# Performance work log

Hardware: AMD Instinct MI355X
Metric: run time of the kernel (lower is better)

The kernel has to match this reference:

```python
import jax, jax.numpy as jnp
import numpy as np

B, C_IN, C_OUT, K, H, W = 8, 64, 64, 3, 128, 128
CTX = max(8, C_OUT // 4)  # 16


def setup_inputs() -> dict:
    key = jax.random.key(0)
    ks = jax.random.split(key, 6)
    x = jax.random.normal(ks[0], (B, C_IN, H, W), dtype=jnp.float32)
    # context_proj: 1x1 conv (ctx_ch, C_in) + bias
    ctx_w = jax.random.normal(ks[1], (CTX, C_IN), dtype=jnp.float32) * (1.0 / np.sqrt(C_IN))
    ctx_b = jnp.zeros((CTX,), dtype=jnp.float32)
    # kernel_gen: Linear(ctx_ch -> C_out*C_in*K*K), init std=0.001, zero bias
    kg_w = jax.random.normal(ks[2], (C_OUT * C_IN * K * K, CTX), dtype=jnp.float32) * 0.001
    kg_b = jnp.zeros((C_OUT * C_IN * K * K,), dtype=jnp.float32)
    gamma = jnp.zeros((C_OUT,), dtype=jnp.float32)
    bias = jnp.zeros((C_OUT,), dtype=jnp.float32)
    # value_proj: 1x1 conv (C_in, C_in), no bias
    value_w = jax.random.normal(ks[3], (C_IN, C_IN), dtype=jnp.float32) * (1.0 / np.sqrt(C_IN))
    return {"x": x, "ctx_w": ctx_w, "ctx_b": ctx_b, "kg_w": kg_w, "kg_b": kg_b,
            "gamma": gamma, "bias": bias, "value_w": value_w}


def reference(x, ctx_w, ctx_b, kg_w, kg_b, gamma, bias, value_w):
    b = x.shape[0]
    # context projection (1x1 conv) + global average pool -> (B, CTX)
    ctx = jnp.einsum('bchw,oc->bohw', x, ctx_w) + ctx_b[None, :, None, None]
    ctx_vec = jnp.mean(ctx, axis=(2, 3))  # (B, CTX)
    # per-sample kernel generation
    kernels_flat = ctx_vec @ kg_w.T + kg_b  # (B, O*C*K*K)
    kernels = jnp.tanh(kernels_flat.reshape(b, C_OUT, C_IN, K, K))
    mean_k = jnp.mean(kernels.reshape(b, C_OUT, -1), axis=-1)  # (B, O)
    lam = jax.nn.sigmoid(gamma)[None, :, None, None, None]
    kernels = kernels - lam * mean_k[:, :, None, None, None]
    # value projection (1x1 conv, no bias)
    v = jnp.einsum('bchw,oc->bohw', x, value_w)
    # unfold: patches (B, C*K*K, H, W), feature order (C, kh, kw) matching F.unfold
    pad = K // 2
    patches = jax.lax.conv_general_dilated_patches(
        v, filter_shape=(K, K), window_strides=(1, 1),
        padding=[(pad, pad), (pad, pad)])  # (B, C*K*K, H, W)
    out = jnp.einsum('bof,bfhw->bohw', kernels.reshape(b, C_OUT, -1), patches)
    out = out + bias[None, :, None, None]
    return jax.nn.relu(out)
```

## Files before the change

### kernel.cpp

```cpp
#include <hip/hip_runtime.h>
#include <stdint.h>

#define NB 8
#define CIN 64
#define COUT 64
#define HH 128
#define WW 128

typedef unsigned short ushort_t;
typedef unsigned int uint_t;
typedef __attribute__((ext_vector_type(8))) __bf16 bf16x8;
typedef __attribute__((ext_vector_type(4))) float f32x4;

__device__ __forceinline__ ushort_t f2bf(float f) {
  uint_t u = __builtin_bit_cast(uint_t, f);
  u += 0x7fffu + ((u >> 16) & 1u);
  return (ushort_t)(u >> 16);
}

#define WS_PART 0
#define WS_XT   262144
#define WS_A    17039360

__global__ void k_trans(const float* __restrict__ x, ushort_t* __restrict__ xT,
                        float* __restrict__ part) {
  __shared__ float tile[64 * 129];
  int b = blockIdx.x >> 7;
  int h = blockIdx.x & 127;
  int tid = threadIdx.x;
  int w = tid & 127;
  int ch = tid >> 7;
  const float* xp = x + ((size_t)(b * 64) * 128 + h) * 128 + w;
#pragma unroll
  for (int p = 0; p < 32; ++p) {
    int c = p * 2 + ch;
    tile[c * 129 + w] = xp[(size_t)c * 16384];
  }
  __syncthreads();
  if (tid < 64) {
    float s = 0.f;
#pragma unroll 8
    for (int w2 = 0; w2 < 128; ++w2) s += tile[tid * 129 + w2];
    part[((size_t)b * 128 + h) * 64 + tid] = s;
  }
#pragma unroll
  for (int it = 0; it < 4; ++it) {
    int chunk = tid + it * 256;
    int w2 = chunk >> 3;
    int cc = chunk & 7;
    union { ushort_t u[8]; int4 v; } pk;
#pragma unroll
    for (int j = 0; j < 8; ++j) pk.u[j] = f2bf(tile[(cc * 8 + j) * 129 + w2]);
    *reinterpret_cast<int4*>(xT + (((size_t)(b * 128 + h) * 128 + w2) * 64 + cc * 8)) = pk.v;
  }
}

__global__ void k_gen(const float* __restrict__ part,
                      const float* __restrict__ ctx_w, const float* __restrict__ ctx_b,
                      const float* __restrict__ kg_w, const float* __restrict__ kg_b,
                      const float* __restrict__ gamma, const float* __restrict__ value_w,
                      ushort_t* __restrict__ A) {
  __shared__ float xm[64];
  __shared__ float ctxv[16];
  __shared__ float ks_[576];
  __shared__ float red[256];
  __shared__ float vw[4096];
  int b = blockIdx.x >> 6;
  int o = blockIdx.x & 63;
  int tid = threadIdx.x;
  {
    int c = tid & 63;
    int g = tid >> 6;
    float s = 0.f;
    const float* pp = part + ((size_t)b * 128 + g * 32) * 64 + c;
#pragma unroll 8
    for (int h = 0; h < 32; ++h) s += pp[h * 64];
    red[tid] = s;
  }
#pragma unroll
  for (int p = 0; p < 16; ++p) vw[tid + p * 256] = value_w[tid + p * 256];
  __syncthreads();
  if (tid < 64)
    xm[tid] = (red[tid] + red[tid + 64] + red[tid + 128] + red[tid + 192]) * (1.f / 16384.f);
  __syncthreads();
  if (tid < 16) {
    float s = ctx_b[tid];
#pragma unroll 8
    for (int c = 0; c < 64; ++c) s += xm[c] * ctx_w[tid * 64 + c];
    ctxv[tid] = s;
  }
  __syncthreads();
  float val[3] = {0.f, 0.f, 0.f};
  float partial = 0.f;
#pragma unroll
  for (int p = 0; p < 3; ++p) {
    int i = tid + p * 256;
    if (i < 576) {
      int n = o * 576 + i;
      float s = kg_b[n];
      const float* kwp = kg_w + (size_t)n * 16;
#pragma unroll
      for (int j = 0; j < 16; ++j) s += ctxv[j] * kwp[j];
      val[p] = tanhf(s);
      partial += val[p];
    }
  }
  __syncthreads();
  red[tid] = partial;
  __syncthreads();
  for (int s = 128; s > 0; s >>= 1) {
    if (tid < s) red[tid] += red[tid + s];
    __syncthreads();
  }
  float mean = red[0] * (1.f / 576.f);
  float lam = 1.f / (1.f + expf(-gamma[o]));
#pragma unroll
  for (int p = 0; p < 3; ++p) {
    int i = tid + p * 256;
    if (i < 576) ks_[i] = val[p] - lam * mean;
  }
  __syncthreads();
  ushort_t* Ao = A + (size_t)(b * 64 + o) * 576;
#pragma unroll
  for (int p = 0; p < 3; ++p) {
    int f = tid + p * 256;
    if (f < 576) {
      int tap = f >> 6;
      int c = f & 63;
      float s = 0.f;
#pragma unroll 8
      for (int cp = 0; cp < 64; ++cp) s += ks_[cp * 9 + tap] * vw[cp * 64 + c];
      Ao[f] = f2bf(s);
    }
  }
}

__launch_bounds__(256, 2)
__global__ void k_conv(const ushort_t* __restrict__ xT, const ushort_t* __restrict__ A,
                       const float* __restrict__ bias, float* __restrict__ out) {
  __shared__ __align__(16) ushort_t xs[6 * 34 * 72];
  int bx = blockIdx.x;
  int b = bx >> 7;
  int rem = bx & 127;
  int h0 = (rem >> 2) * 4;
  int w0 = (rem & 3) * 32;
  int tid = threadIdx.x;
  int wave = tid >> 6;
  int lane = tid & 63;
  int n16 = lane & 15;
  int q = lane >> 4;
  int p  = wave & 1;
  int oh = wave >> 1;

  bf16x8 af[2][18];
#pragma unroll
  for (int t = 0; t < 2; ++t) {
    const ushort_t* Ag = A + (size_t)(b * 64 + oh * 32 + t * 16 + n16) * 576 + q * 8;
#pragma unroll
    for (int ks = 0; ks < 18; ++ks)
      af[t][ks] = *reinterpret_cast<const bf16x8*>(Ag + ks * 32);
  }

  const ushort_t* xb = xT + (size_t)b * 128 * 128 * 64;
#pragma unroll
  for (int it = 0; it < 7; ++it) {
    int chunk = tid + it * 256;
    if (chunk < 1632) {
      int lr = chunk / 272;
      int r2 = chunk - lr * 272;
      int lc = r2 >> 3;
      int cc = r2 & 7;
      int hh = h0 - 1 + lr;
      int ww = w0 - 1 + lc;
      int4 v = make_int4(0, 0, 0, 0);
      if (hh >= 0 && hh < 128 && ww >= 0 && ww < 128)
        v = *reinterpret_cast<const int4*>(xb + ((size_t)(hh * 128 + ww) * 64 + cc * 8));
      *reinterpret_cast<int4*>(xs + ((lr * 34 + lc) * 72 + cc * 8)) = v;
    }
  }
  __syncthreads();

  f32x4 acc[4][2];
#pragma unroll
  for (int i = 0; i < 4; ++i)
#pragma unroll
    for (int t = 0; t < 2; ++t) acc[i][t] = (f32x4){0.f, 0.f, 0.f, 0.f};

  const ushort_t* xsl = xs + n16 * 72 + q * 8;
#pragma unroll
  for (int pt = 0; pt < 4; ++pt) {
    int nt = p * 4 + pt;
    int rr = nt >> 1, cb = nt & 1;
#pragma unroll
    for (int tap = 0; tap < 9; ++tap) {
      int kh = tap / 3, kw2 = tap % 3;
#pragma unroll
      for (int cq = 0; cq < 2; ++cq) {
        bf16x8 bf = *reinterpret_cast<const bf16x8*>(
            xsl + ((rr + kh) * 34 + cb * 16 + kw2) * 72 + cq * 32);
        int ks = tap * 2 + cq;
        acc[pt][0] = __builtin_amdgcn_mfma_f32_16x16x32_bf16(af[0][ks], bf, acc[pt][0], 0, 0, 0);
        acc[pt][1] = __builtin_amdgcn_mfma_f32_16x16x32_bf16(af[1][ks], bf, acc[pt][1], 0, 0, 0);
      }
    }
  }

#pragma unroll
  for (int pt = 0; pt < 4; ++pt) {
    int nt = p * 4 + pt;
    int rr = nt >> 1, cb = nt & 1;
    int hcur = h0 + rr;
    int wcur = w0 + cb * 16 + n16;
#pragma unroll
    for (int t = 0; t < 2; ++t) {
#pragma unroll
      for (int r = 0; r < 4; ++r) {
        int o = oh * 32 + t * 16 + q * 4 + r;
        float v = acc[pt][t][r] + bias[o];
        v = fmaxf(v, 0.f);
        out[((size_t)(b * 64 + o) * 128 + hcur) * 128 + wcur] = v;
      }
    }
  }
}

extern "C" void kernel_launch(void* const* d_in, const int* in_sizes, int n_in,
                              void* d_out, int out_size, void* d_ws, size_t ws_size,
                              hipStream_t stream) {
  const float* x       = (const float*)d_in[0];
  const float* ctx_w   = (const float*)d_in[1];
  const float* ctx_b   = (const float*)d_in[2];
  const float* kg_w    = (const float*)d_in[3];
  const float* kg_b    = (const float*)d_in[4];
  const float* gamma   = (const float*)d_in[5];
  const float* bias    = (const float*)d_in[6];
  const float* value_w = (const float*)d_in[7];
  float* out = (float*)d_out;

  float* part  = (float*)((char*)d_ws + WS_PART);
  ushort_t* xT = (ushort_t*)((char*)d_ws + WS_XT);
  ushort_t* A  = (ushort_t*)((char*)d_ws + WS_A);

  k_trans<<<1024, 256, 0, stream>>>(x, xT, part);
  k_gen<<<512, 256, 0, stream>>>(part, ctx_w, ctx_b, kg_w, kg_b, gamma, value_w, A);
  k_conv<<<1024, 256, 0, stream>>>(xT, A, bias, out);
}
```

Measured before the change: 132.0 us.

## Drop bf16 NHWC transpose pass; convert fp32 NCHW directly into LDS in conv

Removes the k_trans kernel that wrote a bf16 channels-last copy of x. A simple per-(b,c) mean-reduction kernel replaces it, and k_conv now reads fp32 NCHW x directly, packs channel pairs to bf16 and writes them into the shared tile, with separate loads for the halo columns. This removes a 16 MB intermediate write and its reread. The cost is more, narrower global loads in the conv kernel (4-byte strided per-channel reads) and conversion work repeated across overlapping tiles. It also leaves a dead no-op block behind.

Measured after the change: 154.9 us. 17.3% more time.

```diff
diff --git a/kernel.cpp b/kernel.cpp
--- a/kernel.cpp
+++ b/kernel.cpp
@@ -18,44 +18,30 @@
   return (ushort_t)(u >> 16);
 }
 
-#define WS_PART 0
-#define WS_XT   262144
-#define WS_A    17039360
-
-__global__ void k_trans(const float* __restrict__ x, ushort_t* __restrict__ xT,
-                        float* __restrict__ part) {
-  __shared__ float tile[64 * 129];
-  int b = blockIdx.x >> 7;
-  int h = blockIdx.x & 127;
+#define WS_A    0
+#define WS_XSUM 589824
+
+__global__ void k_mean(const float* __restrict__ x, float* __restrict__ xsum) {
+  __shared__ float red[256];
+  int bc = blockIdx.x;
   int tid = threadIdx.x;
-  int w = tid & 127;
-  int ch = tid >> 7;
-  const float* xp = x + ((size_t)(b * 64) * 128 + h) * 128 + w;
-#pragma unroll
-  for (int p = 0; p < 32; ++p) {
-    int c = p * 2 + ch;
-    tile[c * 129 + w] = xp[(size_t)c * 16384];
-  }
-  __syncthreads();
-  if (tid < 64) {
-    float s = 0.f;
-#pragma unroll 8
-    for (int w2 = 0; w2 < 128; ++w2) s += tile[tid * 129 + w2];
-    part[((size_t)b * 128 + h) * 64 + tid] = s;
-  }
-#pragma unroll
-  for (int it = 0; it < 4; ++it) {
-    int chunk = tid + it * 256;
-    int w2 = chunk >> 3;
-    int cc = chunk & 7;
-    union { ushort_t u[8]; int4 v; } pk;
-#pragma unroll
-    for (int j = 0; j < 8; ++j) pk.u[j] = f2bf(tile[(cc * 8 + j) * 129 + w2]);
-    *reinterpret_cast<int4*>(xT + (((size_t)(b * 128 + h) * 128 + w2) * 64 + cc * 8)) = pk.v;
-  }
-}
-
-__global__ void k_gen(const float* __restrict__ part,
+  const float4* xp4 = (const float4*)(x + (size_t)bc * 16384);
+  float s = 0.f;
+#pragma unroll
+  for (int i = 0; i < 16; ++i) {
+    float4 v = xp4[tid + i * 256];
+    s += (v.x + v.y) + (v.z + v.w);
+  }
+  red[tid] = s;
+  __syncthreads();
+  for (int st = 128; st > 0; st >>= 1) {
+    if (tid < st) red[tid] += red[tid + st];
+    __syncthreads();
+  }
+  if (tid == 0) xsum[bc] = red[0];
+}
+
+__global__ void k_gen(const float* __restrict__ xsum,
                       const float* __restrict__ ctx_w, const float* __restrict__ ctx_b,
                       const float* __restrict__ kg_w, const float* __restrict__ kg_b,
                       const float* __restrict__ gamma, const float* __restrict__ value_w,
@@ -68,20 +54,9 @@
   int b = blockIdx.x >> 6;
   int o = blockIdx.x & 63;
   int tid = threadIdx.x;
-  {
-    int c = tid & 63;
-    int g = tid >> 6;
-    float s = 0.f;
-    const float* pp = part + ((size_t)b * 128 + g * 32) * 64 + c;
-#pragma unroll 8
-    for (int h = 0; h < 32; ++h) s += pp[h * 64];
-    red[tid] = s;
-  }
+  if (tid < 64) xm[tid] = xsum[b * 64 + tid] * (1.f / 16384.f);
 #pragma unroll
   for (int p = 0; p < 16; ++p) vw[tid + p * 256] = value_w[tid + p * 256];
-  __syncthreads();
-  if (tid < 64)
-    xm[tid] = (red[tid] + red[tid + 64] + red[tid + 128] + red[tid + 192]) * (1.f / 16384.f);
   __syncthreads();
   if (tid < 16) {
     float s = ctx_b[tid];
@@ -105,7 +80,6 @@
       partial += val[p];
     }
   }
-  __syncthreads();
   red[tid] = partial;
   __syncthreads();
   for (int s = 128; s > 0; s >>= 1) {
@@ -136,7 +110,7 @@
 }
 
 __launch_bounds__(256, 2)
-__global__ void k_conv(const ushort_t* __restrict__ xT, const ushort_t* __restrict__ A,
+__global__ void k_conv(const float* __restrict__ x, const ushort_t* __restrict__ A,
                        const float* __restrict__ bias, float* __restrict__ out) {
   __shared__ __align__(16) ushort_t xs[6 * 34 * 72];
   int bx = blockIdx.x;
@@ -161,21 +135,46 @@
       af[t][ks] = *reinterpret_cast<const bf16x8*>(Ag + ks * 32);
   }
 
-  const ushort_t* xb = xT + (size_t)b * 128 * 128 * 64;
-#pragma unroll
-  for (int it = 0; it < 7; ++it) {
+  const float* xb = x + (size_t)b * 64 * 16384;
+#pragma unroll
+  for (int it = 0; it < 24; ++it) {
     int chunk = tid + it * 256;
-    if (chunk < 1632) {
-      int lr = chunk / 272;
-      int r2 = chunk - lr * 272;
-      int lc = r2 >> 3;
-      int cc = r2 & 7;
+    int lcp = chunk & 31;
+    int cp  = (chunk >> 5) & 31;
+    int lr  = chunk >> 10;
+    int hh = h0 - 1 + lr;
+    int ww = w0 + lcp;
+    uint_t pk = 0;
+    if (hh >= 0 && hh < 128) {
+      const float* src = xb + ((size_t)(2 * cp) * 128 + hh) * 128 + ww;
+      float f0 = src[0];
+      float f1 = src[16384];
+      pk = (uint_t)f2bf(f0) | ((uint_t)f2bf(f1) << 16);
+    }
+    *reinterpret_cast<uint_t*>(xs + (lr * 34 + (lcp + 1)) * 72 + 2 * cp) = pk;
+  }
+  {
+    int chunk = tid + ((tid < 128) ? 256 : 0);
+  }
+#pragma unroll
+  for (int it = 0; it < 2; ++it) {
+    int chunk = tid + it * 256;
+    if (chunk < 384) {
+      int side = chunk & 1;
+      int rest = chunk >> 1;
+      int cp = rest & 31;
+      int lr = rest >> 5;
+      int lc = side ? 33 : 0;
       int hh = h0 - 1 + lr;
       int ww = w0 - 1 + lc;
-      int4 v = make_int4(0, 0, 0, 0);
-      if (hh >= 0 && hh < 128 && ww >= 0 && ww < 128)
-        v = *reinterpret_cast<const int4*>(xb + ((size_t)(hh * 128 + ww) * 64 + cc * 8));
-      *reinterpret_cast<int4*>(xs + ((lr * 34 + lc) * 72 + cc * 8)) = v;
+      uint_t pk = 0;
+      if (hh >= 0 && hh < 128 && ww >= 0 && ww < 128) {
+        const float* src = xb + ((size_t)(2 * cp) * 128 + hh) * 128 + ww;
+        float f0 = src[0];
+        float f1 = src[16384];
+        pk = (uint_t)f2bf(f0) | ((uint_t)f2bf(f1) << 16);
+      }
+      *reinterpret_cast<uint_t*>(xs + (lr * 34 + lc) * 72 + 2 * cp) = pk;
     }
   }
   __syncthreads();
@@ -237,11 +236,10 @@
   const float* value_w = (const float*)d_in[7];
   float* out = (float*)d_out;
 
-  float* part  = (float*)((char*)d_ws + WS_PART);
-  ushort_t* xT = (ushort_t*)((char*)d_ws + WS_XT);
   ushort_t* A  = (ushort_t*)((char*)d_ws + WS_A);
-
-  k_trans<<<1024, 256, 0, stream>>>(x, xT, part);
-  k_gen<<<512, 256, 0, stream>>>(part, ctx_w, ctx_b, kg_w, kg_b, gamma, value_w, A);
-  k_conv<<<1024, 256, 0, stream>>>(xT, A, bias, out);
-}
+  float* xsum  = (float*)((char*)d_ws + WS_XSUM);
+
+  k_mean<<<512, 256, 0, stream>>>(x, xsum);
+  k_gen<<<512, 256, 0, stream>>>(xsum, ctx_w, ctx_b, kg_w, kg_b, gamma, value_w, A);
+  k_conv<<<1024, 256, 0, stream>>>(x, A, bias, out);
+}
```

## Pre-pad transposed input, stream A fragments per row, stage output through LDS

Applied to the files above, without the earlier changes.

The transpose kernel now writes a zero-padded 130x130 layout, with extra blocks zeroing the border rows, so the conv halo load needs no bounds checks. The conv kernel stops holding all 36 A fragments in registers and reloads 12 per kernel row inside a non-unrolled loop. It raises launch bounds from 2 to 4 blocks per SIMD. The epilogue stages results through shared memory so each output row is written as coalesced float4 stores. The cost is repeated A loads from global or cache, extra barriers in the epilogue, and a larger workspace.

After: 130.9 us. About the same (-0.9%).

```diff
diff --git a/kernel.cpp b/kernel.cpp
--- a/kernel.cpp
+++ b/kernel.cpp
@@ -20,14 +20,23 @@
 
 #define WS_PART 0
 #define WS_XT   262144
-#define WS_A    17039360
-
-__global__ void k_trans(const float* __restrict__ x, ushort_t* __restrict__ xT,
+#define WS_A    17567744
+
+__global__ void k_trans(const float* __restrict__ x, ushort_t* __restrict__ xTp,
                         float* __restrict__ part) {
+  int bx = blockIdx.x;
+  int tid = threadIdx.x;
+  if (bx >= 1024) {
+    int j = bx - 1024;
+    int b = j >> 1;
+    int row = (j & 1) ? 129 : 0;
+    int4* dst = reinterpret_cast<int4*>(xTp + ((size_t)b * 130 + row) * 130 * 64);
+    for (int it = tid; it < 1040; it += 256) dst[it] = make_int4(0, 0, 0, 0);
+    return;
+  }
   __shared__ float tile[64 * 129];
-  int b = blockIdx.x >> 7;
-  int h = blockIdx.x & 127;
-  int tid = threadIdx.x;
+  int b = bx >> 7;
+  int h = bx & 127;
   int w = tid & 127;
   int ch = tid >> 7;
   const float* xp = x + ((size_t)(b * 64) * 128 + h) * 128 + w;
@@ -43,6 +52,13 @@
     for (int w2 = 0; w2 < 128; ++w2) s += tile[tid * 129 + w2];
     part[((size_t)b * 128 + h) * 64 + tid] = s;
   }
+  if (tid < 16) {
+    int col = (tid < 8) ? 0 : 129;
+    int cc = tid & 7;
+    *reinterpret_cast<int4*>(xTp + (((size_t)b * 130 + h + 1) * 130 + col) * 64 + cc * 8) =
+        make_int4(0, 0, 0, 0);
+  }
+  ushort_t* dst = xTp + (((size_t)b * 130 + h + 1) * 130 + 1) * 64;
 #pragma unroll
   for (int it = 0; it < 4; ++it) {
     int chunk = tid + it * 256;
@@ -51,7 +67,7 @@
     union { ushort_t u[8]; int4 v; } pk;
 #pragma unroll
     for (int j = 0; j < 8; ++j) pk.u[j] = f2bf(tile[(cc * 8 + j) * 129 + w2]);
-    *reinterpret_cast<int4*>(xT + (((size_t)(b * 128 + h) * 128 + w2) * 64 + cc * 8)) = pk.v;
+    *reinterpret_cast<int4*>(dst + (size_t)w2 * 64 + cc * 8) = pk.v;
   }
 }
 
@@ -135,33 +151,26 @@
   }
 }
 
-__launch_bounds__(256, 2)
-__global__ void k_conv(const ushort_t* __restrict__ xT, const ushort_t* __restrict__ A,
+__launch_bounds__(256, 4)
+__global__ void k_conv(const ushort_t* __restrict__ xTp, const ushort_t* __restrict__ A,
                        const float* __restrict__ bias, float* __restrict__ out) {
   __shared__ __align__(16) ushort_t xs[6 * 34 * 72];
+  float* buf = reinterpret_cast<float*>(xs);
+
   int bx = blockIdx.x;
   int b = bx >> 7;
   int rem = bx & 127;
-  int h0 = (rem >> 2) * 4;
-  int w0 = (rem & 3) * 32;
+  int h0 = (rem >> 2) << 2;
+  int w0 = (rem & 3) << 5;
   int tid = threadIdx.x;
+  int lane = tid & 63;
   int wave = tid >> 6;
-  int lane = tid & 63;
   int n16 = lane & 15;
   int q = lane >> 4;
-  int p  = wave & 1;
+  int p = wave & 1;
   int oh = wave >> 1;
 
-  bf16x8 af[2][18];
-#pragma unroll
-  for (int t = 0; t < 2; ++t) {
-    const ushort_t* Ag = A + (size_t)(b * 64 + oh * 32 + t * 16 + n16) * 576 + q * 8;
-#pragma unroll
-    for (int ks = 0; ks < 18; ++ks)
-      af[t][ks] = *reinterpret_cast<const bf16x8*>(Ag + ks * 32);
-  }
-
-  const ushort_t* xb = xT + (size_t)b * 128 * 128 * 64;
+  const ushort_t* xb = xTp + (size_t)b * (130 * 130 * 64);
 #pragma unroll
   for (int it = 0; it < 7; ++it) {
     int chunk = tid + it * 256;
@@ -170,12 +179,9 @@
       int r2 = chunk - lr * 272;
       int lc = r2 >> 3;
       int cc = r2 & 7;
-      int hh = h0 - 1 + lr;
-      int ww = w0 - 1 + lc;
-      int4 v = make_int4(0, 0, 0, 0);
-      if (hh >= 0 && hh < 128 && ww >= 0 && ww < 128)
-        v = *reinterpret_cast<const int4*>(xb + ((size_t)(hh * 128 + ww) * 64 + cc * 8));
-      *reinterpret_cast<int4*>(xs + ((lr * 34 + lc) * 72 + cc * 8)) = v;
+      int4 v = *reinterpret_cast<const int4*>(
+          xb + ((size_t)(h0 + lr) * 130 + (w0 + lc)) * 64 + cc * 8);
+      *reinterpret_cast<int4*>(xs + (lr * 34 + lc) * 72 + cc * 8) = v;
     }
   }
   __syncthreads();
@@ -186,40 +192,67 @@
 #pragma unroll
     for (int t = 0; t < 2; ++t) acc[i][t] = (f32x4){0.f, 0.f, 0.f, 0.f};
 
-  const ushort_t* xsl = xs + n16 * 72 + q * 8;
-#pragma unroll
-  for (int pt = 0; pt < 4; ++pt) {
-    int nt = p * 4 + pt;
-    int rr = nt >> 1, cb = nt & 1;
-#pragma unroll
-    for (int tap = 0; tap < 9; ++tap) {
-      int kh = tap / 3, kw2 = tap % 3;
-#pragma unroll
-      for (int cq = 0; cq < 2; ++cq) {
-        bf16x8 bf = *reinterpret_cast<const bf16x8*>(
-            xsl + ((rr + kh) * 34 + cb * 16 + kw2) * 72 + cq * 32);
-        int ks = tap * 2 + cq;
-        acc[pt][0] = __builtin_amdgcn_mfma_f32_16x16x32_bf16(af[0][ks], bf, acc[pt][0], 0, 0, 0);
-        acc[pt][1] = __builtin_amdgcn_mfma_f32_16x16x32_bf16(af[1][ks], bf, acc[pt][1], 0, 0, 0);
+  const ushort_t* Ag0 = A + (size_t)(b * 64 + oh * 32 + n16) * 576 + q * 8;
+  const ushort_t* Ag1 = Ag0 + 16 * 576;
+  const ushort_t* xslk = xs + (p * 2) * (34 * 72) + n16 * 72 + q * 8;
+
+#pragma unroll 1
+  for (int kh = 0; kh < 3; ++kh) {
+    bf16x8 a0[6], a1[6];
+#pragma unroll
+    for (int i = 0; i < 6; ++i) {
+      a0[i] = *reinterpret_cast<const bf16x8*>(Ag0 + i * 32);
+      a1[i] = *reinterpret_cast<const bf16x8*>(Ag1 + i * 32);
+    }
+#pragma unroll
+    for (int pt = 0; pt < 4; ++pt) {
+      int rloc = pt >> 1;
+      int colb = (pt & 1) * 16;
+#pragma unroll
+      for (int kw2 = 0; kw2 < 3; ++kw2) {
+#pragma unroll
+        for (int cq = 0; cq < 2; ++cq) {
+          bf16x8 bv = *reinterpret_cast<const bf16x8*>(
+              xslk + (rloc * 34 + colb + kw2) * 72 + cq * 32);
+          int i = kw2 * 2 + cq;
+          acc[pt][0] = __builtin_amdgcn_mfma_f32_16x16x32_bf16(a0[i], bv, acc[pt][0], 0, 0, 0);
+          acc[pt][1] = __builtin_amdgcn_mfma_f32_16x16x32_bf16(a1[i], bv, acc[pt][1], 0, 0, 0);
+        }
       }
     }
-  }
-
-#pragma unroll
-  for (int pt = 0; pt < 4; ++pt) {
-    int nt = p * 4 + pt;
-    int rr = nt >> 1, cb = nt & 1;
-    int hcur = h0 + rr;
-    int wcur = w0 + cb * 16 + n16;
-#pragma unroll
-    for (int t = 0; t < 2; ++t) {
-#pragma unroll
-      for (int r = 0; r < 4; ++r) {
-        int o = oh * 32 + t * 16 + q * 4 + r;
-        float v = acc[pt][t][r] + bias[o];
-        v = fmaxf(v, 0.f);
-        out[((size_t)(b * 64 + o) * 128 + hcur) * 128 + wcur] = v;
+    Ag0 += 192;
+    Ag1 += 192;
+    xslk += 34 * 72;
+  }
+
+  f32x4 bias0 = *reinterpret_cast<const f32x4*>(bias + oh * 32 + q * 4);
+  f32x4 bias1 = *reinterpret_cast<const f32x4*>(bias + oh * 32 + 16 + q * 4);
+
+#pragma unroll
+  for (int rr = 0; rr < 4; ++rr) {
+    __syncthreads();
+    if ((rr >> 1) == p) {
+      int ptb = (rr & 1) * 2;
+#pragma unroll
+      for (int cb = 0; cb < 2; ++cb) {
+        int pt = ptb + cb;
+        int w = cb * 16 + n16;
+#pragma unroll
+        for (int r = 0; r < 4; ++r) {
+          buf[(oh * 32 + q * 4 + r) * 36 + w] = fmaxf(acc[pt][0][r] + bias0[r], 0.f);
+          buf[(oh * 32 + 16 + q * 4 + r) * 36 + w] = fmaxf(acc[pt][1][r] + bias1[r], 0.f);
+        }
       }
+    }
+    __syncthreads();
+    float* op = out + ((size_t)(b * 64) * 128 + (h0 + rr)) * 128 + w0;
+#pragma unroll
+    for (int k = 0; k < 2; ++k) {
+      int idx = tid + k * 256;
+      int o = idx >> 3;
+      int wq = idx & 7;
+      f32x4 v = *reinterpret_cast<f32x4*>(buf + o * 36 + wq * 4);
+      *reinterpret_cast<f32x4*>(op + (size_t)o * 16384 + wq * 4) = v;
     }
   }
 }
@@ -238,10 +271,10 @@
   float* out = (float*)d_out;
 
   float* part  = (float*)((char*)d_ws + WS_PART);
-  ushort_t* xT = (ushort_t*)((char*)d_ws + WS_XT);
+  ushort_t* xTp = (ushort_t*)((char*)d_ws + WS_XT);
   ushort_t* A  = (ushort_t*)((char*)d_ws + WS_A);
 
-  k_trans<<<1024, 256, 0, stream>>>(x, xT, part);
+  k_trans<<<1040, 256, 0, stream>>>(x, xTp, part);
   k_gen<<<512, 256, 0, stream>>>(part, ctx_w, ctx_b, kg_w, kg_b, gamma, value_w, A);
-  k_conv<<<1024, 256, 0, stream>>>(xT, A, bias, out);
-}
+  k_conv<<<1024, 256, 0, stream>>>(xTp, A, bias, out);
+}
```
